# Optimization experiments

Measured on AMD Instinct MI355X. Metric: run time of the kernel, lower is better.

Reference implementation:

```python
import jax, jax.numpy as jnp
import numpy as np

N_NODES = 100000
N_EDGES = 1600000
IN_FEATS, HIDDEN, OUT = 128, 128, 1


def setup_inputs() -> dict:
    key = jax.random.key(0)
    ks = jax.random.split(key, 5)
    x = jax.random.normal(ks[0], (N_NODES, IN_FEATS), dtype=jnp.float32)
    src = jax.random.randint(ks[1], (N_EDGES,), 0, N_NODES, dtype=jnp.int64)
    dst = jax.random.randint(ks[2], (N_EDGES,), 0, N_NODES, dtype=jnp.int64)
    W1 = jax.random.normal(ks[3], (IN_FEATS, HIDDEN), dtype=jnp.float32) * 0.05
    b1 = jnp.zeros((HIDDEN,), dtype=jnp.float32)
    W2 = jax.random.normal(ks[4], (HIDDEN, OUT), dtype=jnp.float32) * 0.05
    b2 = jnp.zeros((OUT,), dtype=jnp.float32)
    return {"x": x, "src": src, "dst": dst, "W1": W1, "b1": b1, "W2": W2, "b2": b2}


def reference(x, src, dst, W1, b1, W2, b2):
    n = x.shape[0]
    ones = jnp.ones(src.shape[0], dtype=x.dtype)
    # DGL GraphConv norm='both': symmetric normalization, degrees clamped at 1
    inv_sqrt_out = jnp.clip(jax.ops.segment_sum(ones, src, num_segments=n), 1.0) ** -0.5
    inv_sqrt_in = jnp.clip(jax.ops.segment_sum(ones, dst, num_segments=n), 1.0) ** -0.5

    def graph_conv(h, W, b):
        # out = D_in^{-1/2} A D_out^{-1/2} h W + b ; project first (shrinks edge traffic)
        h = (h * inv_sqrt_out[:, None]) @ W            # [N, d_out]
        agg = jax.ops.segment_sum(h[src], dst, num_segments=n)  # sparse SpMM
        return agg * inv_sqrt_in[:, None] + b

    h = jax.nn.relu(graph_conv(x, W1, b1))
    return graph_conv(h, W2, b2)
```

## Files before the change

### kernel.cpp

```cpp
#include <hip/hip_runtime.h>
#include <hip/hip_bf16.h>

#define NF 128
#define EPB 4096
#define EPB2 8192
#define CAP 6144

typedef __attribute__((ext_vector_type(8))) short short8;
typedef __attribute__((ext_vector_type(4))) float f32x4;
typedef __attribute__((ext_vector_type(4))) unsigned int uint4e;

__global__ void k_init(int* __restrict__ bucketCnt, int* __restrict__ bucketCntS,
                       int* __restrict__ rowoff, int N, int E) {
  int i = threadIdx.x;
  for (int k = i; k < 512; k += 256) { bucketCnt[k] = 0; bucketCntS[k] = 0; }
  if (i == 0) rowoff[N] = E;
}

__global__ __launch_bounds__(256) void k_frontA(const int* __restrict__ src,
                                                const int* __restrict__ dst,
                                                const float* __restrict__ W1,
                                                int* __restrict__ bucketCnt,
                                                int* __restrict__ bucketCntS,
                                                int2* __restrict__ region,
                                                int* __restrict__ regionS,
                                                unsigned short* __restrict__ WbT,
                                                int E, int B1, int B2) {
  __shared__ __align__(16) char smem_raw[42240];
  int* cnt   = (int*)smem_raw;
  int* scanv = cnt + 512;
  int* cur   = scanv + 512;
  int* gb    = cur + 512;
  int* s1    = gb + 512;
  void* stv  = (void*)(smem_raw + 9216 + 256);
  int tid = threadIdx.x;
  int b = blockIdx.x;

  if (b >= B1 + B2) {
    int u = (b - B1 - B2) * 256 + tid;
    int n  = u >> 5;
    int k4 = (u & 31) << 2;
    ushort4 o;
    __hip_bfloat16 h0 = __float2bfloat16(W1[(k4 + 0) * NF + n]);
    __hip_bfloat16 h1 = __float2bfloat16(W1[(k4 + 1) * NF + n]);
    __hip_bfloat16 h2 = __float2bfloat16(W1[(k4 + 2) * NF + n]);
    __hip_bfloat16 h3 = __float2bfloat16(W1[(k4 + 3) * NF + n]);
    o.x = *(unsigned short*)&h0;
    o.y = *(unsigned short*)&h1;
    o.z = *(unsigned short*)&h2;
    o.w = *(unsigned short*)&h3;
    *(ushort4*)&WbT[n * NF + k4] = o;
    return;
  }

  if (b < B1) {
    int2* st = (int2*)stv;
    int b0 = b * EPB;
    int n = E - b0; if (n > EPB) n = EPB;

    for (int k = tid; k < 512; k += 256) cnt[k] = 0;
    __syncthreads();
    for (int k = tid; k < n; k += 256) atomicAdd(&cnt[dst[b0 + k] >> 8], 1);
    __syncthreads();

    int c0 = cnt[2 * tid], c1 = cnt[2 * tid + 1];
    s1[tid] = c0 + c1;
    __syncthreads();
    for (int off = 1; off < 256; off <<= 1) {
      int v = (tid >= off) ? s1[tid - off] : 0;
      __syncthreads();
      s1[tid] += v;
      __syncthreads();
    }
    int excl = tid ? s1[tid - 1] : 0;
    scanv[2 * tid] = excl;
    scanv[2 * tid + 1] = excl + c0;
    cur[2 * tid] = excl;
    cur[2 * tid + 1] = excl + c0;
    gb[2 * tid]     = c0 ? atomicAdd(&bucketCnt[2 * tid], c0) : 0;
    gb[2 * tid + 1] = c1 ? atomicAdd(&bucketCnt[2 * tid + 1], c1) : 0;
    __syncthreads();

    for (int k = tid; k < n; k += 256) {
      int d = dst[b0 + k], s = src[b0 + k];
      int p = atomicAdd(&cur[d >> 8], 1);
      st[p] = make_int2(d, s);
    }
    __syncthreads();
    for (int k = tid; k < n; k += 256) {
      int2 e = st[k];
      int bk = e.x >> 8;
      int gp = gb[bk] + (k - scanv[bk]);
      if (gp < CAP) region[(size_t)bk * CAP + gp] = e;
    }
    return;
  }

  int* st = (int*)stv;
  int b0 = (b - B1) * EPB2;
  int n = E - b0; if (n > EPB2) n = EPB2;

  for (int k = tid; k < 512; k += 256) cnt[k] = 0;
  __syncthreads();
  for (int k = tid; k < n; k += 256) atomicAdd(&cnt[src[b0 + k] >> 8], 1);
  __syncthreads();

  int c0 = cnt[2 * tid], c1 = cnt[2 * tid + 1];
  s1[tid] = c0 + c1;
  __syncthreads();
  for (int off = 1; off < 256; off <<= 1) {
    int v = (tid >= off) ? s1[tid - off] : 0;
    __syncthreads();
    s1[tid] += v;
    __syncthreads();
  }
  int excl = tid ? s1[tid - 1] : 0;
  scanv[2 * tid] = excl;
  scanv[2 * tid + 1] = excl + c0;
  cur[2 * tid] = excl;
  cur[2 * tid + 1] = excl + c0;
  gb[2 * tid]     = c0 ? atomicAdd(&bucketCntS[2 * tid], c0) : 0;
  gb[2 * tid + 1] = c1 ? atomicAdd(&bucketCntS[2 * tid + 1], c1) : 0;
  __syncthreads();

  for (int k = tid; k < n; k += 256) {
    int s = src[b0 + k];
    int p = atomicAdd(&cur[s >> 8], 1);
    st[p] = s;
  }
  __syncthreads();
  for (int k = tid; k < n; k += 256) {
    int s = st[k];
    int bk = s >> 8;
    int gp = gb[bk] + (k - scanv[bk]);
    if (gp < CAP) regionS[(size_t)bk * CAP + gp] = s;
  }
}

__global__ __launch_bounds__(256) void k_mid(const float* __restrict__ x,
                                             const unsigned short* __restrict__ WbT,
                                             const int2* __restrict__ region,
                                             const int* __restrict__ bucketCnt,
                                             const int* __restrict__ regionS,
                                             const int* __restrict__ bucketCntS,
                                             int* __restrict__ csr,
                                             int* __restrict__ rowoff,
                                             float* __restrict__ invI,
                                             float* __restrict__ invO,
                                             unsigned short* __restrict__ xw,
                                             int N, int NB) {
  __shared__ __align__(16) char smem_raw[52224];
  int tid = threadIdx.x;
  int blk = blockIdx.x;

  if (blk < NB) {
    int* s1   = (int*)smem_raw;
    int* hist = s1 + 256;
    int* incl = hist + 256;
    int* cur  = incl + 256;
    int b = blk;
    int c0 = (2 * tid < NB) ? bucketCnt[2 * tid] : 0;
    int c1 = (2 * tid + 1 < NB) ? bucketCnt[2 * tid + 1] : 0;
    s1[tid] = c0 + c1;
    __syncthreads();
    for (int off = 1; off < 256; off <<= 1) {
      int v = (tid >= off) ? s1[tid - off] : 0;
      __syncthreads();
      s1[tid] += v;
      __syncthreads();
    }
    int t = b >> 1;
    int csrBase = t ? s1[t - 1] : 0;
    if (b & 1) csrBase += bucketCnt[b & ~1];

    int base = b << 8;
    int nN = N - base; if (nN > 256) nN = 256;
    int cntb = bucketCnt[b]; if (cntb > CAP) cntb = CAP;
    const int2* reg = region + (size_t)b * CAP;

    hist[tid] = 0;
    __syncthreads();
    for (int k = tid; k < cntb; k += 256) atomicAdd(&hist[reg[k].x - base], 1);
    __syncthreads();
    int h = hist[tid];
    incl[tid] = h;
    __syncthreads();
    for (int off = 1; off < 256; off <<= 1) {
      int v = (tid >= off) ? incl[tid - off] : 0;
      __syncthreads();
      incl[tid] += v;
      __syncthreads();
    }
    int startt = incl[tid] - h;
    if (tid < nN) {
      rowoff[base + tid] = csrBase + startt;
      invI[base + tid] = rsqrtf(fmaxf((float)h, 1.0f));
    }
    cur[tid] = startt;
    __syncthreads();
    for (int k = tid; k < cntb; k += 256) {
      int2 e = reg[k];
      int p = atomicAdd(&cur[e.x - base], 1);
      csr[csrBase + p] = e.y;
    }
    return;
  }

  if (blk < 2 * NB) {
    int* hist = (int*)smem_raw;
    int b = blk - NB;
    int base = b << 8;
    int cntb = bucketCntS[b]; if (cntb > CAP) cntb = CAP;
    const int* reg = regionS + (size_t)b * CAP;
    hist[tid] = 0;
    __syncthreads();
    for (int k = tid; k < cntb; k += 256) atomicAdd(&hist[reg[k] - base], 1);
    __syncthreads();
    if (base + tid < N) invO[base + tid] = rsqrtf(fmaxf((float)hist[tid], 1.0f));
    return;
  }

  unsigned short* Wb = (unsigned short*)smem_raw;
  unsigned short* Xb = Wb + 128 * 136;
  int idx = blk - 2 * NB;
  int rowbase = idx * 64;

  for (int t = tid; t < 64 * 32; t += 256) {
    int r = t >> 5, k4 = (t & 31) << 2;
    int row = rowbase + r; if (row >= N) row = N - 1;
    float4 v = *(const float4*)&x[(size_t)row * NF + k4];
    __hip_bfloat16 h0 = __float2bfloat16(v.x);
    __hip_bfloat16 h1 = __float2bfloat16(v.y);
    __hip_bfloat16 h2 = __float2bfloat16(v.z);
    __hip_bfloat16 h3 = __float2bfloat16(v.w);
    ushort4 u;
    u.x = *(unsigned short*)&h0;
    u.y = *(unsigned short*)&h1;
    u.z = *(unsigned short*)&h2;
    u.w = *(unsigned short*)&h3;
    *(ushort4*)&Xb[r * 136 + k4] = u;
  }
  for (int t = tid; t < 128 * 16; t += 256) {
    int n = t >> 4, k8 = (t & 15) << 3;
    short8 v = *(const short8*)&WbT[n * NF + k8];
    *(short8*)&Wb[n * 136 + k8] = v;
  }
  __syncthreads();

  int w    = tid >> 6;
  int lane = tid & 63;
  int r16  = lane & 15;
  int kg   = lane >> 4;

  short8 afrag[4];
#pragma unroll
  for (int kk = 0; kk < 4; ++kk) {
    afrag[kk] = *(const short8*)&Xb[(w * 16 + r16) * 136 + kg * 8 + kk * 32];
  }

#pragma unroll
  for (int ct = 0; ct < 8; ++ct) {
    f32x4 acc = {0.f, 0.f, 0.f, 0.f};
#pragma unroll
    for (int kk = 0; kk < 4; ++kk) {
      short8 bfrag = *(const short8*)&Wb[(ct * 16 + r16) * 136 + kg * 8 + kk * 32];
      acc = __builtin_amdgcn_mfma_f32_16x16x32_bf16(afrag[kk], bfrag, acc, 0, 0, 0);
    }
#pragma unroll
    for (int reg = 0; reg < 4; ++reg) {
      int row = rowbase + w * 16 + kg * 4 + reg;
      if (row < N) {
        __hip_bfloat16 hb = __float2bfloat16(acc[reg]);
        xw[(size_t)row * NF + ct * 16 + r16] = *(unsigned short*)&hb;
      }
    }
  }
}

__global__ __launch_bounds__(256) void k_gather_proj(const unsigned short* __restrict__ xw,
                                                     const int* __restrict__ rowoff,
                                                     const int* __restrict__ csr,
                                                     const float* __restrict__ invI,
                                                     const float* __restrict__ invO,
                                                     const float* __restrict__ b1,
                                                     const float* __restrict__ W2,
                                                     float* __restrict__ h2, int N) {
  int i    = blockIdx.x * 4 + (threadIdx.x >> 6);
  int lane = threadIdx.x & 63;
  int grp  = lane >> 4;
  int sl   = lane & 15;
  if (i >= N) return;
  int jb = rowoff[i];
  int je = rowoff[i + 1];
  const uint4e* xwq = (const uint4e*)xw;
  float a0 = 0.f, a1 = 0.f, a2 = 0.f, a3 = 0.f;
  float a4 = 0.f, a5 = 0.f, a6 = 0.f, a7 = 0.f;

#define ACC8(v, o)                                                         \
  do {                                                                     \
    a0 = fmaf(__uint_as_float(((v).x & 0xffffu) << 16), (o), a0);          \
    a1 = fmaf(__uint_as_float((v).x & 0xffff0000u), (o), a1);              \
    a2 = fmaf(__uint_as_float(((v).y & 0xffffu) << 16), (o), a2);          \
    a3 = fmaf(__uint_as_float((v).y & 0xffff0000u), (o), a3);              \
    a4 = fmaf(__uint_as_float(((v).z & 0xffffu) << 16), (o), a4);          \
    a5 = fmaf(__uint_as_float((v).z & 0xffff0000u), (o), a5);              \
    a6 = fmaf(__uint_as_float(((v).w & 0xffffu) << 16), (o), a6);          \
    a7 = fmaf(__uint_as_float((v).w & 0xffff0000u), (o), a7);              \
  } while (0)

  int j = jb;
  for (; j + 8 <= je; j += 8) {
    int s0 = csr[j + grp];
    int s1 = csr[j + 4 + grp];
    float o0 = invO[s0], o1 = invO[s1];
    uint4e v0 = xwq[(size_t)s0 * 16 + sl];
    uint4e v1 = xwq[(size_t)s1 * 16 + sl];
    ACC8(v0, o0);
    ACC8(v1, o1);
  }
  for (; j < je; j += 4) {
    int e = j + grp;
    if (e < je) {
      int s = csr[e];
      float o = invO[s];
      uint4e v = xwq[(size_t)s * 16 + sl];
      ACC8(v, o);
    }
  }
#undef ACC8

  a0 += __shfl_xor(a0, 16); a0 += __shfl_xor(a0, 32);
  a1 += __shfl_xor(a1, 16); a1 += __shfl_xor(a1, 32);
  a2 += __shfl_xor(a2, 16); a2 += __shfl_xor(a2, 32);
  a3 += __shfl_xor(a3, 16); a3 += __shfl_xor(a3, 32);
  a4 += __shfl_xor(a4, 16); a4 += __shfl_xor(a4, 32);
  a5 += __shfl_xor(a5, 16); a5 += __shfl_xor(a5, 32);
  a6 += __shfl_xor(a6, 16); a6 += __shfl_xor(a6, 32);
  a7 += __shfl_xor(a7, 16); a7 += __shfl_xor(a7, 32);

  float inI = invI[i];
  int f = sl * 8;
  float4 bl = *(const float4*)&b1[f];
  float4 bh = *(const float4*)&b1[f + 4];
  float4 wl = *(const float4*)&W2[f];
  float4 wh = *(const float4*)&W2[f + 4];
  float p = fmaxf(fmaf(a0, inI, bl.x), 0.f) * wl.x
          + fmaxf(fmaf(a1, inI, bl.y), 0.f) * wl.y
          + fmaxf(fmaf(a2, inI, bl.z), 0.f) * wl.z
          + fmaxf(fmaf(a3, inI, bl.w), 0.f) * wl.w
          + fmaxf(fmaf(a4, inI, bh.x), 0.f) * wh.x
          + fmaxf(fmaf(a5, inI, bh.y), 0.f) * wh.y
          + fmaxf(fmaf(a6, inI, bh.z), 0.f) * wh.z
          + fmaxf(fmaf(a7, inI, bh.w), 0.f) * wh.w;
#pragma unroll
  for (int off = 8; off; off >>= 1) p += __shfl_xor(p, off);
  if (lane == 0) h2[i] = p * invO[i];
}

__global__ __launch_bounds__(256) void k_gather2(const float* __restrict__ h2,
                                                 const int* __restrict__ rowoff,
                                                 const int* __restrict__ csr,
                                                 const float* __restrict__ invI,
                                                 const float* __restrict__ b2,
                                                 float* __restrict__ out, int N) {
  int i = blockIdx.x * 64 + (threadIdx.x >> 2);
  int q = threadIdx.x & 3;
  if (i >= N) return;
  int jb = rowoff[i];
  int je = rowoff[i + 1];
  float s = 0.f;
  for (int j = jb + q; j < je; j += 4) s += h2[csr[j]];
  s += __shfl_xor(s, 1);
  s += __shfl_xor(s, 2);
  if (q == 0) out[i] = s * invI[i] + b2[0];
}

extern "C" void kernel_launch(void* const* d_in, const int* in_sizes, int n_in,
                              void* d_out, int out_size, void* d_ws, size_t ws_size,
                              hipStream_t stream) {
  const float* x   = (const float*)d_in[0];
  const int*   src = (const int*)d_in[1];
  const int*   dst = (const int*)d_in[2];
  const float* W1  = (const float*)d_in[3];
  const float* b1  = (const float*)d_in[4];
  const float* W2  = (const float*)d_in[5];
  const float* b2  = (const float*)d_in[6];
  int N = in_sizes[0] / NF;
  int E = in_sizes[1];
  int NB = (N + 255) >> 8;

  int* bucketCnt  = (int*)d_ws;
  int* bucketCntS = bucketCnt + 512;
  unsigned short* WbT = (unsigned short*)(bucketCntS + 512);
  int* rowoff     = (int*)(WbT + NF * NF);
  int* csr        = rowoff + (size_t)N + 8;
  int2* region    = (int2*)(csr + (size_t)E);
  int* regionS    = (int*)(region + (size_t)NB * CAP);
  float* invO     = (float*)(regionS + (size_t)NB * CAP);
  float* invI     = invO + N;
  float* h2       = invI + N;
  unsigned short* xw = (unsigned short*)(h2 + N);
  float* out      = (float*)d_out;

  int B1 = (E + EPB - 1) / EPB;
  int B2 = (E + EPB2 - 1) / EPB2;
  int BW = 16;
  int G  = (N + 63) / 64;

  k_init<<<1, 256, 0, stream>>>(bucketCnt, bucketCntS, rowoff, N, E);
  k_frontA<<<B1 + B2 + BW, 256, 0, stream>>>(src, dst, W1, bucketCnt, bucketCntS,
                                             region, regionS, WbT, E, B1, B2);
  k_mid<<<2 * NB + G, 256, 0, stream>>>(x, WbT, region, bucketCnt, regionS, bucketCntS,
                                        csr, rowoff, invI, invO, xw, N, NB);
  k_gather_proj<<<(N + 3) / 4, 256, 0, stream>>>(xw, rowoff, csr, invI, invO, b1, W2, h2, N);
  k_gather2<<<(N + 63) / 64, 256, 0, stream>>>(h2, rowoff, csr, invI, b2, out, N);
}
```

Baseline: 169.8 us.

## Move X@W1 projection into edge-bucketing kernel and split CSR build out

Result: faster. 163.1 us (-3.9%).

```diff
diff --git a/kernel.cpp b/kernel.cpp
--- a/kernel.cpp
+++ b/kernel.cpp
@@ -10,51 +10,54 @@
 typedef __attribute__((ext_vector_type(4))) float f32x4;
 typedef __attribute__((ext_vector_type(4))) unsigned int uint4e;
 
-__global__ void k_init(int* __restrict__ bucketCnt, int* __restrict__ bucketCntS,
-                       int* __restrict__ rowoff, int N, int E) {
-  int i = threadIdx.x;
-  for (int k = i; k < 512; k += 256) { bucketCnt[k] = 0; bucketCntS[k] = 0; }
-  if (i == 0) rowoff[N] = E;
-}
-
-__global__ __launch_bounds__(256) void k_frontA(const int* __restrict__ src,
-                                                const int* __restrict__ dst,
-                                                const float* __restrict__ W1,
-                                                int* __restrict__ bucketCnt,
-                                                int* __restrict__ bucketCntS,
-                                                int2* __restrict__ region,
-                                                int* __restrict__ regionS,
-                                                unsigned short* __restrict__ WbT,
-                                                int E, int B1, int B2) {
-  __shared__ __align__(16) char smem_raw[42240];
-  int* cnt   = (int*)smem_raw;
-  int* scanv = cnt + 512;
-  int* cur   = scanv + 512;
-  int* gb    = cur + 512;
-  int* s1    = gb + 512;
-  void* stv  = (void*)(smem_raw + 9216 + 256);
+__global__ __launch_bounds__(256) void k_init(const float* __restrict__ W1,
+                                              int* __restrict__ bucketCnt,
+                                              int* __restrict__ bucketCntS,
+                                              int* __restrict__ rowoff,
+                                              unsigned short* __restrict__ WbT,
+                                              int N, int E) {
   int tid = threadIdx.x;
   int b = blockIdx.x;
-
-  if (b >= B1 + B2) {
-    int u = (b - B1 - B2) * 256 + tid;
-    int n  = u >> 5;
-    int k4 = (u & 31) << 2;
-    ushort4 o;
-    __hip_bfloat16 h0 = __float2bfloat16(W1[(k4 + 0) * NF + n]);
-    __hip_bfloat16 h1 = __float2bfloat16(W1[(k4 + 1) * NF + n]);
-    __hip_bfloat16 h2 = __float2bfloat16(W1[(k4 + 2) * NF + n]);
-    __hip_bfloat16 h3 = __float2bfloat16(W1[(k4 + 3) * NF + n]);
-    o.x = *(unsigned short*)&h0;
-    o.y = *(unsigned short*)&h1;
-    o.z = *(unsigned short*)&h2;
-    o.w = *(unsigned short*)&h3;
-    *(ushort4*)&WbT[n * NF + k4] = o;
-    return;
-  }
+  if (b == 0) {
+    for (int k = tid; k < 512; k += 256) { bucketCnt[k] = 0; bucketCntS[k] = 0; }
+    if (tid == 0) rowoff[N] = E;
+  }
+  int u = b * 256 + tid;
+  int n  = u >> 5;
+  int k4 = (u & 31) << 2;
+  ushort4 o;
+  __hip_bfloat16 h0 = __float2bfloat16(W1[(k4 + 0) * NF + n]);
+  __hip_bfloat16 h1 = __float2bfloat16(W1[(k4 + 1) * NF + n]);
+  __hip_bfloat16 h2 = __float2bfloat16(W1[(k4 + 2) * NF + n]);
+  __hip_bfloat16 h3 = __float2bfloat16(W1[(k4 + 3) * NF + n]);
+  o.x = *(unsigned short*)&h0;
+  o.y = *(unsigned short*)&h1;
+  o.z = *(unsigned short*)&h2;
+  o.w = *(unsigned short*)&h3;
+  *(ushort4*)&WbT[n * NF + k4] = o;
+}
+
+__global__ __launch_bounds__(256) void k_front(const float* __restrict__ x,
+                                               const int* __restrict__ src,
+                                               const int* __restrict__ dst,
+                                               const unsigned short* __restrict__ WbT,
+                                               int* __restrict__ bucketCnt,
+                                               int* __restrict__ bucketCntS,
+                                               int2* __restrict__ region,
+                                               int* __restrict__ regionS,
+                                               unsigned short* __restrict__ xw,
+                                               int N, int E, int B1, int B2) {
+  __shared__ __align__(16) char smem_raw[52224];
+  int tid = threadIdx.x;
+  int b = blockIdx.x;
 
   if (b < B1) {
-    int2* st = (int2*)stv;
+    int* cnt   = (int*)smem_raw;
+    int* scanv = cnt + 512;
+    int* cur   = scanv + 512;
+    int* gb    = cur + 512;
+    int* s1    = gb + 512;
+    int2* st   = (int2*)(smem_raw + 9216 + 256);
     int b0 = b * EPB;
     int n = E - b0; if (n > EPB) n = EPB;
 
@@ -96,71 +99,22 @@
     return;
   }
 
-  int* st = (int*)stv;
-  int b0 = (b - B1) * EPB2;
-  int n = E - b0; if (n > EPB2) n = EPB2;
-
-  for (int k = tid; k < 512; k += 256) cnt[k] = 0;
-  __syncthreads();
-  for (int k = tid; k < n; k += 256) atomicAdd(&cnt[src[b0 + k] >> 8], 1);
-  __syncthreads();
-
-  int c0 = cnt[2 * tid], c1 = cnt[2 * tid + 1];
-  s1[tid] = c0 + c1;
-  __syncthreads();
-  for (int off = 1; off < 256; off <<= 1) {
-    int v = (tid >= off) ? s1[tid - off] : 0;
-    __syncthreads();
-    s1[tid] += v;
-    __syncthreads();
-  }
-  int excl = tid ? s1[tid - 1] : 0;
-  scanv[2 * tid] = excl;
-  scanv[2 * tid + 1] = excl + c0;
-  cur[2 * tid] = excl;
-  cur[2 * tid + 1] = excl + c0;
-  gb[2 * tid]     = c0 ? atomicAdd(&bucketCntS[2 * tid], c0) : 0;
-  gb[2 * tid + 1] = c1 ? atomicAdd(&bucketCntS[2 * tid + 1], c1) : 0;
-  __syncthreads();
-
-  for (int k = tid; k < n; k += 256) {
-    int s = src[b0 + k];
-    int p = atomicAdd(&cur[s >> 8], 1);
-    st[p] = s;
-  }
-  __syncthreads();
-  for (int k = tid; k < n; k += 256) {
-    int s = st[k];
-    int bk = s >> 8;
-    int gp = gb[bk] + (k - scanv[bk]);
-    if (gp < CAP) regionS[(size_t)bk * CAP + gp] = s;
-  }
-}
-
-__global__ __launch_bounds__(256) void k_mid(const float* __restrict__ x,
-                                             const unsigned short* __restrict__ WbT,
-                                             const int2* __restrict__ region,
-                                             const int* __restrict__ bucketCnt,
-                                             const int* __restrict__ regionS,
-                                             const int* __restrict__ bucketCntS,
-                                             int* __restrict__ csr,
-                                             int* __restrict__ rowoff,
-                                             float* __restrict__ invI,
-                                             float* __restrict__ invO,
-                                             unsigned short* __restrict__ xw,
-                                             int N, int NB) {
-  __shared__ __align__(16) char smem_raw[52224];
-  int tid = threadIdx.x;
-  int blk = blockIdx.x;
-
-  if (blk < NB) {
-    int* s1   = (int*)smem_raw;
-    int* hist = s1 + 256;
-    int* incl = hist + 256;
-    int* cur  = incl + 256;
-    int b = blk;
-    int c0 = (2 * tid < NB) ? bucketCnt[2 * tid] : 0;
-    int c1 = (2 * tid + 1 < NB) ? bucketCnt[2 * tid + 1] : 0;
+  if (b < B1 + B2) {
+    int* cnt   = (int*)smem_raw;
+    int* scanv = cnt + 512;
+    int* cur   = scanv + 512;
+    int* gb    = cur + 512;
+    int* s1    = gb + 512;
+    int* st    = (int*)(smem_raw + 9216 + 256);
+    int b0 = (b - B1) * EPB2;
+    int n = E - b0; if (n > EPB2) n = EPB2;
+
+    for (int k = tid; k < 512; k += 256) cnt[k] = 0;
+    __syncthreads();
+    for (int k = tid; k < n; k += 256) atomicAdd(&cnt[src[b0 + k] >> 8], 1);
+    __syncthreads();
+
+    int c0 = cnt[2 * tid], c1 = cnt[2 * tid + 1];
     s1[tid] = c0 + c1;
     __syncthreads();
     for (int off = 1; off < 256; off <<= 1) {
@@ -169,60 +123,33 @@
       s1[tid] += v;
       __syncthreads();
     }
-    int t = b >> 1;
-    int csrBase = t ? s1[t - 1] : 0;
-    if (b & 1) csrBase += bucketCnt[b & ~1];
-
-    int base = b << 8;
-    int nN = N - base; if (nN > 256) nN = 256;
-    int cntb = bucketCnt[b]; if (cntb > CAP) cntb = CAP;
-    const int2* reg = region + (size_t)b * CAP;
-
-    hist[tid] = 0;
-    __syncthreads();
-    for (int k = tid; k < cntb; k += 256) atomicAdd(&hist[reg[k].x - base], 1);
-    __syncthreads();
-    int h = hist[tid];
-    incl[tid] = h;
-    __syncthreads();
-    for (int off = 1; off < 256; off <<= 1) {
-      int v = (tid >= off) ? incl[tid - off] : 0;
-      __syncthreads();
-      incl[tid] += v;
-      __syncthreads();
-    }
-    int startt = incl[tid] - h;
-    if (tid < nN) {
-      rowoff[base + tid] = csrBase + startt;
-      invI[base + tid] = rsqrtf(fmaxf((float)h, 1.0f));
-    }
-    cur[tid] = startt;
-    __syncthreads();
-    for (int k = tid; k < cntb; k += 256) {
-      int2 e = reg[k];
-      int p = atomicAdd(&cur[e.x - base], 1);
-      csr[csrBase + p] = e.y;
-    }
-    return;
-  }
-
-  if (blk < 2 * NB) {
-    int* hist = (int*)smem_raw;
-    int b = blk - NB;
-    int base = b << 8;
-    int cntb = bucketCntS[b]; if (cntb > CAP) cntb = CAP;
-    const int* reg = regionS + (size_t)b * CAP;
-    hist[tid] = 0;
-    __syncthreads();
-    for (int k = tid; k < cntb; k += 256) atomicAdd(&hist[reg[k] - base], 1);
-    __syncthreads();
-    if (base + tid < N) invO[base + tid] = rsqrtf(fmaxf((float)hist[tid], 1.0f));
+    int excl = tid ? s1[tid - 1] : 0;
+    scanv[2 * tid] = excl;
+    scanv[2 * tid + 1] = excl + c0;
+    cur[2 * tid] = excl;
+    cur[2 * tid + 1] = excl + c0;
+    gb[2 * tid]     = c0 ? atomicAdd(&bucketCntS[2 * tid], c0) : 0;
+    gb[2 * tid + 1] = c1 ? atomicAdd(&bucketCntS[2 * tid + 1], c1) : 0;
+    __syncthreads();
+
+    for (int k = tid; k < n; k += 256) {
+      int s = src[b0 + k];
+      int p = atomicAdd(&cur[s >> 8], 1);
+      st[p] = s;
+    }
+    __syncthreads();
+    for (int k = tid; k < n; k += 256) {
+      int s = st[k];
+      int bk = s >> 8;
+      int gp = gb[bk] + (k - scanv[bk]);
+      if (gp < CAP) regionS[(size_t)bk * CAP + gp] = s;
+    }
     return;
   }
 
   unsigned short* Wb = (unsigned short*)smem_raw;
   unsigned short* Xb = Wb + 128 * 136;
-  int idx = blk - 2 * NB;
+  int idx = b - B1 - B2;
   int rowbase = idx * 64;
 
   for (int t = tid; t < 64 * 32; t += 256) {
@@ -275,6 +202,79 @@
       }
     }
   }
+}
+
+__global__ __launch_bounds__(256) void k_mid2(const int2* __restrict__ region,
+                                              const int* __restrict__ bucketCnt,
+                                              const int* __restrict__ regionS,
+                                              const int* __restrict__ bucketCntS,
+                                              int* __restrict__ csr,
+                                              int* __restrict__ rowoff,
+                                              float* __restrict__ invI,
+                                              float* __restrict__ invO,
+                                              int N, int NB) {
+  __shared__ int s1[256], hist[256], incl[256], cur[256];
+  int tid = threadIdx.x;
+  int blk = blockIdx.x;
+
+  if (blk < NB) {
+    int b = blk;
+    int c0 = (2 * tid < NB) ? bucketCnt[2 * tid] : 0;
+    int c1 = (2 * tid + 1 < NB) ? bucketCnt[2 * tid + 1] : 0;
+    s1[tid] = c0 + c1;
+    __syncthreads();
+    for (int off = 1; off < 256; off <<= 1) {
+      int v = (tid >= off) ? s1[tid - off] : 0;
+      __syncthreads();
+      s1[tid] += v;
+      __syncthreads();
+    }
+    int t = b >> 1;
+    int csrBase = t ? s1[t - 1] : 0;
+    if (b & 1) csrBase += bucketCnt[b & ~1];
+
+    int base = b << 8;
+    int nN = N - base; if (nN > 256) nN = 256;
+    int cntb = bucketCnt[b]; if (cntb > CAP) cntb = CAP;
+    const int2* reg = region + (size_t)b * CAP;
+
+    hist[tid] = 0;
+    __syncthreads();
+    for (int k = tid; k < cntb; k += 256) atomicAdd(&hist[reg[k].x - base], 1);
+    __syncthreads();
+    int h = hist[tid];
+    incl[tid] = h;
+    __syncthreads();
+    for (int off = 1; off < 256; off <<= 1) {
+      int v = (tid >= off) ? incl[tid - off] : 0;
+      __syncthreads();
+      incl[tid] += v;
+      __syncthreads();
+    }
+    int startt = incl[tid] - h;
+    if (tid < nN) {
+      rowoff[base + tid] = csrBase + startt;
+      invI[base + tid] = rsqrtf(fmaxf((float)h, 1.0f));
+    }
+    cur[tid] = startt;
+    __syncthreads();
+    for (int k = tid; k < cntb; k += 256) {
+      int2 e = reg[k];
+      int p = atomicAdd(&cur[e.x - base], 1);
+      csr[csrBase + p] = e.y;
+    }
+    return;
+  }
+
+  int b = blk - NB;
+  int base = b << 8;
+  int cntb = bucketCntS[b]; if (cntb > CAP) cntb = CAP;
+  const int* reg = regionS + (size_t)b * CAP;
+  hist[tid] = 0;
+  __syncthreads();
+  for (int k = tid; k < cntb; k += 256) atomicAdd(&hist[reg[k] - base], 1);
+  __syncthreads();
+  if (base + tid < N) invO[base + tid] = rsqrtf(fmaxf((float)hist[tid], 1.0f));
 }
 
 __global__ __launch_bounds__(256) void k_gather_proj(const unsigned short* __restrict__ xw,
@@ -404,14 +404,13 @@
 
   int B1 = (E + EPB - 1) / EPB;
   int B2 = (E + EPB2 - 1) / EPB2;
-  int BW = 16;
   int G  = (N + 63) / 64;
 
-  k_init<<<1, 256, 0, stream>>>(bucketCnt, bucketCntS, rowoff, N, E);
-  k_frontA<<<B1 + B2 + BW, 256, 0, stream>>>(src, dst, W1, bucketCnt, bucketCntS,
-                                             region, regionS, WbT, E, B1, B2);
-  k_mid<<<2 * NB + G, 256, 0, stream>>>(x, WbT, region, bucketCnt, regionS, bucketCntS,
-                                        csr, rowoff, invI, invO, xw, N, NB);
+  k_init<<<16, 256, 0, stream>>>(W1, bucketCnt, bucketCntS, rowoff, WbT, N, E);
+  k_front<<<B1 + B2 + G, 256, 0, stream>>>(x, src, dst, WbT, bucketCnt, bucketCntS,
+                                           region, regionS, xw, N, E, B1, B2);
+  k_mid2<<<2 * NB, 256, 0, stream>>>(region, bucketCnt, regionS, bucketCntS,
+                                     csr, rowoff, invI, invO, N, NB);
   k_gather_proj<<<(N + 3) / 4, 256, 0, stream>>>(xw, rowoff, csr, invI, invO, b1, W2, h2, N);
   k_gather2<<<(N + 63) / 64, 256, 0, stream>>>(h2, rowoff, csr, invI, b2, out, N);
 }
```
